# Kernel optimization log

Hardware: AMD Instinct MI355X
Metric: run time of the kernel (lower is better)

Reference implementation:

```python
import jax, jax.numpy as jnp
import numpy as np

# dims
B, P, H, W = 4, 512, 32, 32
C2 = P // 2            # 256 per-branch channels
HEAD = 4
DH = C2 // HEAD        # 64 head dim
L = H * W              # 1024 tokens
DI = 2 * C2            # 512 mamba d_inner (expand=2)
N = 64                 # d_state
R = (C2 + 15) // 16    # 16 dt_rank
KC = 4                 # d_conv


def setup_inputs() -> dict:
    key = jax.random.key(0)
    ks = jax.random.split(key, 32)
    f32 = jnp.float32
    def nrm(k, shape, s=0.02):
        return jax.random.normal(k, shape, f32) * s
    inp = {}
    inp['x'] = jax.random.normal(ks[0], (B, P, H, W), f32)
    # GambaCell rel-pos + gate conv
    inp['rel_h_c'] = jax.random.normal(ks[1], (1, C2, 1, H), f32)
    inp['rel_w_c'] = jax.random.normal(ks[2], (1, C2, W, 1), f32)
    inp['gate_w'] = nrm(ks[3], (C2, C2, 3))
    inp['gate_b'] = jnp.zeros((C2,), f32)
    # Mamba params
    inp['W_in'] = nrm(ks[4], (2 * DI, C2))
    inp['conv_w'] = nrm(ks[5], (DI, KC), 0.2)
    inp['conv_b'] = jnp.zeros((DI,), f32)
    inp['W_x'] = nrm(ks[6], (R + 2 * N, DI))
    inp['W_dt'] = nrm(ks[7], (DI, R), 0.1)
    inp['b_dt'] = jnp.full((DI,), -4.0, f32)
    inp['A_log'] = jnp.broadcast_to(jnp.log(jnp.arange(1, N + 1, dtype=f32)), (DI, N)).copy()
    inp['D_p'] = jnp.ones((DI,), f32)
    inp['W_out'] = nrm(ks[8], (C2, DI))
    # MHSA params (1x1 convs -> dense)
    inp['Wq'] = nrm(ks[9], (C2, C2)); inp['bq'] = jnp.zeros((C2,), f32)
    inp['Wk'] = nrm(ks[10], (C2, C2)); inp['bk'] = jnp.zeros((C2,), f32)
    inp['Wv'] = nrm(ks[11], (C2, C2)); inp['bv'] = jnp.zeros((C2,), f32)
    inp['rel_h_m'] = jax.random.normal(ks[12], (1, HEAD, DH, 1, H), f32) * 0.02
    inp['rel_w_m'] = jax.random.normal(ks[13], (1, HEAD, DH, W, 1), f32) * 0.02
    inp['reg_qk'] = jax.random.normal(ks[14], (1, L, L), f32)
    inp['reg_v'] = jax.random.normal(ks[15], (1, DH, L), f32)
    # Gating params
    inp['Wa'] = nrm(ks[16], (P, C2)); inp['ba'] = jnp.zeros((P,), f32)
    inp['Wb'] = nrm(ks[17], (P, C2)); inp['bb'] = jnp.zeros((P,), f32)
    inp['Wg'] = nrm(ks[18], (1, P)); inp['bg'] = jnp.zeros((1,), f32)
    return inp


def _silu(t):
    return t * jax.nn.sigmoid(t)


def _conv1x1(w, b, t):  # Conv2d kernel_size=1
    return jnp.einsum('oc,bchw->bohw', w, t) + b[None, :, None, None]


def _mamba(seq, W_in, conv_w, conv_b, W_x, W_dt, b_dt, A_log, D_p, W_out):
    # seq: (B, L, C2)
    Bn = seq.shape[0]
    xz = seq @ W_in.T                       # (B,L,2*DI)
    xi, z = jnp.split(xz, 2, axis=-1)
    # causal depthwise conv1d, kernel 4, left-pad 3, trimmed to L
    xc = jnp.transpose(xi, (0, 2, 1))       # (B,DI,L)
    xp = jnp.pad(xc, ((0, 0), (0, 0), (KC - 1, 0)))
    conv = conv_b[None, :, None]
    for kk in range(KC):
        conv = conv + conv_w[None, :, kk, None] * xp[:, :, kk:kk + L]
    xs = _silu(conv).transpose(0, 2, 1)     # (B,L,DI)
    x_dbl = xs @ W_x.T                      # (B,L,R+2N)
    dt = jax.nn.softplus(x_dbl[..., :R] @ W_dt.T + b_dt)   # (B,L,DI)
    Bm = x_dbl[..., R:R + N]                # (B,L,N)
    Cm = x_dbl[..., R + N:]                 # (B,L,N)
    A = -jnp.exp(A_log)                     # (DI,N)

    def step(h, t):
        dt_t, B_t, C_t, u_t = t             # (B,DI),(B,N),(B,N),(B,DI)
        dA = jnp.exp(dt_t[..., None] * A)   # (B,DI,N)
        h = dA * h + (dt_t * u_t)[..., None] * B_t[:, None, :]
        y = jnp.sum(h * C_t[:, None, :], axis=-1)
        return h, y

    h0 = jnp.zeros((Bn, DI, N), seq.dtype)
    scan_in = (dt.transpose(1, 0, 2), Bm.transpose(1, 0, 2),
               Cm.transpose(1, 0, 2), xs.transpose(1, 0, 2))
    _, ys = jax.lax.scan(step, h0, scan_in)  # (L,B,DI)
    y = ys.transpose(1, 0, 2) + D_p * xs
    y = y * _silu(z)
    return y @ W_out.T                      # (B,L,C2)


def _forward(x, rel_h_c, rel_w_c, gate_w, gate_b, W_in, conv_w, conv_b, W_x,
             W_dt, b_dt, A_log, D_p, W_out, Wq, bq, Wk, bk, Wv, bv,
             rel_h_m, rel_w_m, reg_qk, reg_v, Wa, ba, Wb, bb, Wg, bg):
    Bn = x.shape[0]
    x1, x2 = x[:, :C2], x[:, C2:]
    # --- GambaCell branch ---
    seq = x1.reshape(Bn, C2, L).transpose(0, 2, 1)          # (B,L,C2)
    pos = (rel_h_c + rel_w_c).reshape(1, C2, L).transpose(0, 2, 1)
    seq = seq + pos
    sc = seq.transpose(0, 2, 1)                             # (B,C2,L)
    ctx = jax.nn.sigmoid(
        jax.lax.conv_general_dilated(sc, gate_w, (1,), [(1, 1)],
                                     dimension_numbers=('NCH', 'OIH', 'NCH'))
        + gate_b[None, :, None]).transpose(0, 2, 1)          # (B,L,C2)
    ym = _mamba(seq, W_in, conv_w, conv_b, W_x, W_dt, b_dt, A_log, D_p, W_out)
    # faithful to original: view (B,L,C)->(B,C,H,W) with no permute
    out1 = (ym * ctx).reshape(Bn, C2, H, W)
    # --- MHSA branch ---
    q = _conv1x1(Wq, bq, x2).reshape(Bn, HEAD, DH, L)
    k = _conv1x1(Wk, bk, x2).reshape(Bn, HEAD, DH, L)
    v = _conv1x1(Wv, bv, x2).reshape(Bn, HEAD, DH, L)
    cc = jnp.einsum('bhdi,bhdj->bhij', q, k)                # content-content
    posm = (rel_h_m + rel_w_m).reshape(HEAD, DH, L)
    cp = jnp.einsum('hdi,bhdj->bhij', posm, q)              # position^T @ q
    energy = cc + cp                                         # (B,HEAD,L,L)
    e = jnp.concatenate([energy, jnp.broadcast_to(reg_qk[None], (Bn, 1, L, L))], axis=1)
    vp = jnp.concatenate([v, jnp.broadcast_to(reg_v[None], (Bn, 1, DH, L))], axis=1)
    attn = jax.nn.softmax(e, axis=-1)
    out = jnp.einsum('bndj,bnij->bndi', vp, attn)           # v @ attn^T
    out2 = out[:, :HEAD].reshape(Bn, C2, H, W)
    # --- Gating fusion ---
    a_proj = _conv1x1(Wa, ba, out1)
    b_proj = _conv1x1(Wb, bb, out2)
    ga = jax.nn.sigmoid(_conv1x1(Wg, bg, a_proj))
    gb = jax.nn.sigmoid(_conv1x1(Wg, bg, b_proj))
    return ga * a_proj + gb * b_proj                        # (B,P,H,W)


def reference(x, rel_h_c, rel_w_c, gate_w, gate_b, W_in, conv_w, conv_b, W_x,
              W_dt, b_dt, A_log, D_p, W_out, Wq, bq, Wk, bk, Wv, bv,
              rel_h_m, rel_w_m, reg_qk, reg_v, Wa, ba, Wb, bb, Wg, bg):
    return _forward(x, rel_h_c, rel_w_c, gate_w, gate_b, W_in, conv_w, conv_b,
                    W_x, W_dt, b_dt, A_log, D_p, W_out, Wq, bq, Wk, bk, Wv, bv,
                    rel_h_m, rel_w_m, reg_qk, reg_v, Wa, ba, Wb, bb, Wg, bg)
```

## Files before the change

### kernel.cpp

```cpp
#include <hip/hip_runtime.h>
#include <math.h>

static constexpr int Bn = 4, Pp = 512, C2 = 256, HEAD = 4, DHd = 64;
static constexpr int Ll = 1024, DIi = 512, Nn = 64, Rr = 16, KCc = 4;

#define DEVI __device__ __forceinline__

DEVI float sigf(float x){ return 1.0f/(1.0f+__expf(-x)); }
DEVI float softplusf(float x){ return x > 20.f ? x : log1pf(__expf(x)); }

DEVI unsigned short bfh(float f){
  unsigned int u = __float_as_uint(f);
  return (unsigned short)((u + 0x7FFFu + ((u>>16)&1u)) >> 16);
}
DEVI float bff(unsigned short h){ return __uint_as_float(((unsigned int)h)<<16); }

typedef __attribute__((ext_vector_type(8))) short  bf8v;
typedef __attribute__((ext_vector_type(4))) float  f4v;
typedef __attribute__((ext_vector_type(8))) unsigned short u16x8;

__global__ void k_transpose(const float* __restrict__ x, const float* __restrict__ rh,
                            const float* __restrict__ rw, float* __restrict__ seq,
                            float* __restrict__ x2seq){
  __shared__ float t[32][33];
  int b = blockIdx.z, c0 = blockIdx.y*32, l0 = blockIdx.x*32;
  for (int i = threadIdx.y; i < 32; i += 8)
    t[i][threadIdx.x] = x[((size_t)(b*Pp + c0 + i)*Ll) + l0 + threadIdx.x];
  __syncthreads();
  for (int i = threadIdx.y; i < 32; i += 8){
    int l = l0 + i, c = c0 + threadIdx.x;
    float v = t[threadIdx.x][i];
    if (c < C2){
      float pos = rh[c*32 + (l & 31)] + rw[c*32 + (l >> 5)];
      seq[(size_t)(b*Ll + l)*C2 + c] = v + pos;
    } else {
      x2seq[(size_t)(b*Ll + l)*C2 + (c - C2)] = v;
    }
  }
}

__global__ void __launch_bounds__(256) k_mgemm(
    const float* __restrict__ A, const float* __restrict__ B,
    float* __restrict__ C, const float* __restrict__ bias,
    int M, int N, int K, int lda, int ldb, int ldc, int act)
{
  __shared__ __align__(16) unsigned short Ah[64*40], Al[64*40], Bh[64*40], Bl[64*40];
  int m0 = blockIdx.y*64, n0 = blockIdx.x*64;
  int t = threadIdx.x;
  int w = t >> 6, l = t & 63;
  int g = l >> 4, r = l & 15;
  int row0 = w*16;

  f4v acc[4];
  #pragma unroll
  for (int j=0;j<4;++j) acc[j] = (f4v){0.f,0.f,0.f,0.f};

  int sr = t >> 2;
  int sc = (t & 3) * 8;

  for (int k0 = 0; k0 < K; k0 += 32){
    {
      const float* src = A + (size_t)(m0+sr)*lda + k0 + sc;
      float4 v0 = *(const float4*)(src);
      float4 v1 = *(const float4*)(src+4);
      float f[8] = {v0.x,v0.y,v0.z,v0.w,v1.x,v1.y,v1.z,v1.w};
      u16x8 hv, lv;
      #pragma unroll
      for (int i=0;i<8;++i){
        unsigned short h = bfh(f[i]); hv[i] = h;
        lv[i] = bfh(f[i] - bff(h));
      }
      *(u16x8*)&Ah[sr*40+sc] = hv;
      *(u16x8*)&Al[sr*40+sc] = lv;
    }
    {
      const float* src = B + (size_t)(n0+sr)*ldb + k0 + sc;
      float4 v0 = *(const float4*)(src);
      float4 v1 = *(const float4*)(src+4);
      float f[8] = {v0.x,v0.y,v0.z,v0.w,v1.x,v1.y,v1.z,v1.w};
      u16x8 hv, lv;
      #pragma unroll
      for (int i=0;i<8;++i){
        unsigned short h = bfh(f[i]); hv[i] = h;
        lv[i] = bfh(f[i] - bff(h));
      }
      *(u16x8*)&Bh[sr*40+sc] = hv;
      *(u16x8*)&Bl[sr*40+sc] = lv;
    }
    __syncthreads();
    bf8v a_h = *(const bf8v*)&Ah[(row0+r)*40 + g*8];
    bf8v a_l = *(const bf8v*)&Al[(row0+r)*40 + g*8];
    #pragma unroll
    for (int j=0;j<4;++j){
      bf8v b_h = *(const bf8v*)&Bh[(j*16+r)*40 + g*8];
      bf8v b_l = *(const bf8v*)&Bl[(j*16+r)*40 + g*8];
      acc[j] = __builtin_amdgcn_mfma_f32_16x16x32_bf16(a_h, b_h, acc[j], 0, 0, 0);
      acc[j] = __builtin_amdgcn_mfma_f32_16x16x32_bf16(a_h, b_l, acc[j], 0, 0, 0);
      acc[j] = __builtin_amdgcn_mfma_f32_16x16x32_bf16(a_l, b_h, acc[j], 0, 0, 0);
    }
    __syncthreads();
  }
  #pragma unroll
  for (int j=0;j<4;++j){
    int n = n0 + j*16 + r;
    float bv = bias ? bias[n] : 0.f;
    #pragma unroll
    for (int q=0;q<4;++q){
      int m = m0 + row0 + g*4 + q;
      float v = acc[j][q] + bv;
      if (act == 1) v = sigf(v);
      Cb_write:
      C[(size_t)m*ldc + n] = v;
    }
  }
}

template<int BMODE>
__global__ void __launch_bounds__(256) k_gemm(
       const float* __restrict__ A, const float* __restrict__ B,
       float* __restrict__ C, const float* __restrict__ bias,
       int M, int N, int K, int lda, int ldb, int ldc,
       long sA1, long sA2, long sB1, long sB2, long sC1, long sC2, int act)
{
  __shared__ float As[16][64];
  __shared__ float Bs[16][64];
  int z = blockIdx.z;
  const float* Ab = A + (size_t)((z>>2)*sA1 + (z&3)*sA2);
  const float* Bb = B + (size_t)((z>>2)*sB1 + (z&3)*sB2);
  float*       Cb = C + (size_t)((z>>2)*sC1 + (z&3)*sC2);
  int m0 = blockIdx.y*64, n0 = blockIdx.x*64;
  int t = threadIdx.x, tx = t & 15, ty = t >> 4;
  float acc[4][4] = {};
  int arow = t >> 2, akq = (t & 3) * 4;
  for (int k0 = 0; k0 < K; k0 += 16){
    float4 av = *(const float4*)(Ab + (size_t)(m0+arow)*lda + k0 + akq);
    As[akq+0][arow] = av.x; As[akq+1][arow] = av.y;
    As[akq+2][arow] = av.z; As[akq+3][arow] = av.w;
    if (BMODE == 0){
      float4 bv = make_float4(0.f,0.f,0.f,0.f);
      if (n0 + arow < N) bv = *(const float4*)(Bb + (size_t)(n0+arow)*ldb + k0 + akq);
      Bs[akq+0][arow]=bv.x; Bs[akq+1][arow]=bv.y;
      Bs[akq+2][arow]=bv.z; Bs[akq+3][arow]=bv.w;
    } else {
      int kr = t >> 4, nq = (t & 15) * 4;
      float4 bv = make_float4(0.f,0.f,0.f,0.f);
      if (n0 + nq < N) bv = *(const float4*)(Bb + (size_t)(k0+kr)*ldb + n0 + nq);
      *(float4*)&Bs[kr][nq] = bv;
    }
    __syncthreads();
    #pragma unroll
    for (int k = 0; k < 16; ++k){
      float4 a = *(const float4*)&As[k][ty*4];
      float4 b = *(const float4*)&Bs[k][tx*4];
      acc[0][0] = fmaf(a.x,b.x,acc[0][0]); acc[0][1] = fmaf(a.x,b.y,acc[0][1]);
      acc[0][2] = fmaf(a.x,b.z,acc[0][2]); acc[0][3] = fmaf(a.x,b.w,acc[0][3]);
      acc[1][0] = fmaf(a.y,b.x,acc[1][0]); acc[1][1] = fmaf(a.y,b.y,acc[1][1]);
      acc[1][2] = fmaf(a.y,b.z,acc[1][2]); acc[1][3] = fmaf(a.y,b.w,acc[1][3]);
      acc[2][0] = fmaf(a.z,b.x,acc[2][0]); acc[2][1] = fmaf(a.z,b.y,acc[2][1]);
      acc[2][2] = fmaf(a.z,b.z,acc[2][2]); acc[2][3] = fmaf(a.z,b.w,acc[2][3]);
      acc[3][0] = fmaf(a.w,b.x,acc[3][0]); acc[3][1] = fmaf(a.w,b.y,acc[3][1]);
      acc[3][2] = fmaf(a.w,b.z,acc[3][2]); acc[3][3] = fmaf(a.w,b.w,acc[3][3]);
    }
    __syncthreads();
  }
  #pragma unroll
  for (int i = 0; i < 4; ++i){
    int m = m0 + ty*4 + i;
    #pragma unroll
    for (int j = 0; j < 4; ++j){
      int n = n0 + tx*4 + j;
      if (n < N){
        float v = acc[i][j];
        if (bias) v += bias[n];
        if (act == 1) v = sigf(v);
        else if (act == 2) v = softplusf(v);
        Cb[(size_t)m*ldc + n] = v;
      }
    }
  }
}

__global__ void k_im2col(const float* __restrict__ seq, float* __restrict__ A2){
  int idx = blockIdx.x*256 + threadIdx.x;
  int j  = idx % 768;
  int bl = idx / 768;
  int kk = j >> 8, c = j & 255;
  int l = bl & 1023, b = bl >> 10;
  int ls = l + kk - 1;
  float v = 0.f;
  if (ls >= 0 && ls < Ll) v = seq[(size_t)(b*Ll + ls)*C2 + c];
  A2[idx] = v;
}

__global__ void k_packw(const float* __restrict__ gw, float* __restrict__ W2){
  int idx = blockIdx.x*256 + threadIdx.x;
  int j = idx % 768, o = idx / 768;
  int kk = j >> 8, i = j & 255;
  W2[idx] = gw[(size_t)(o*256 + i)*3 + kk];
}

__global__ void k_dwconv(const float* __restrict__ xz, const float* __restrict__ cw,
                         const float* __restrict__ cb, float* __restrict__ xs){
  int idx = blockIdx.x*256 + threadIdx.x;
  int d = idx & 511; int bl = idx >> 9; int l = bl & 1023; int b = bl >> 10;
  float s = cb[d];
  #pragma unroll
  for (int kk = 0; kk < 4; ++kk){
    int ls = l - 3 + kk;
    if (ls >= 0) s = fmaf(cw[d*4+kk], xz[(size_t)(b*Ll+ls)*1024 + d], s);
  }
  xs[idx] = s * sigf(s);
}

__global__ void __launch_bounds__(64, 2) k_scan2(
    const float* __restrict__ dt, const float* __restrict__ xdbl,
    const float* __restrict__ xs, const float* __restrict__ xz,
    const float* __restrict__ A_log, const float* __restrict__ D_p,
    float* __restrict__ y){
  __shared__ float pbuf[64*65];
  int lane = threadIdx.x;
  int wid  = blockIdx.x;
  int b = wid >> 9, d = wid & 511;
  float Ac = -__expf(A_log[d*64 + lane]);
  float Dp = D_p[d];
  float h = 0.f;
  size_t base = (size_t)b*Ll;
  for (int c0 = 0; c0 < Ll; c0 += 64){
    size_t rowj = base + c0 + lane;
    float dtv = dt[rowj*512 + d];
    float uv  = xs[rowj*512 + d];
    float zv  = xz[rowj*1024 + 512 + d];
    float dtu = dtv*uv;
    float Bv[64], Cv[64];
    #pragma unroll
    for (int l = 0; l < 64; ++l){
      size_t r2 = (base + c0 + l)*144;
      Bv[l] = xdbl[r2 + 16 + lane];
      Cv[l] = xdbl[r2 + 80 + lane];
    }
    #pragma unroll
    for (int l = 0; l < 64; ++l){
      float sdt  = __shfl(dtv, l);
      float sdtu = __shfl(dtu, l);
      float dA = __expf(sdt*Ac);
      h = fmaf(dA, h, sdtu*Bv[l]);
      pbuf[l*65 + lane] = h*Cv[l];
    }
    __syncthreads();
    float s0=0.f, s1=0.f, s2=0.f, s3=0.f;
    const float* rp = &pbuf[lane*65];
    #pragma unroll
    for (int n = 0; n < 64; n += 4){
      s0 += rp[n]; s1 += rp[n+1]; s2 += rp[n+2]; s3 += rp[n+3];
    }
    float p = (s0+s1)+(s2+s3);
    y[rowj*512 + d] = (p + Dp*uv) * (zv * sigf(zv));
    __syncthreads();
  }
}

__global__ void k_pack_ab(const float* __restrict__ qt, const float* __restrict__ kt,
                          const float* __restrict__ rhm, const float* __restrict__ rwm,
                          float* __restrict__ Ab, float* __restrict__ Bb){
  int idx = blockIdx.x*256 + threadIdx.x;
  int dd = idx & 127;
  int i  = (idx >> 7) & 1023;
  int h  = (idx >> 17) & 3;
  int b  = idx >> 19;
  float av, bv;
  if (dd < 64){
    size_t q = (size_t)(b*Ll + i)*C2 + h*64 + dd;
    av = qt[q]; bv = kt[q];
  } else {
    int d = dd - 64;
    av = rhm[(h*64+d)*32 + (i & 31)] + rwm[(h*64+d)*32 + (i >> 5)];
    bv = qt[(size_t)(b*Ll + i)*C2 + h*64 + d];
  }
  Ab[idx] = av; Bb[idx] = bv;
}

__global__ void __launch_bounds__(256) k_softmax(float* __restrict__ e){
  __shared__ float red[4];
  __shared__ float red2[4];
  size_t row = blockIdx.x;
  float* p = e + row*1024;
  int t = threadIdx.x;
  float v0 = p[t], v1 = p[t+256], v2 = p[t+512], v3 = p[t+768];
  float mx = fmaxf(fmaxf(v0,v1), fmaxf(v2,v3));
  #pragma unroll
  for (int off=32; off; off>>=1) mx = fmaxf(mx, __shfl_xor(mx, off));
  if ((t&63)==0) red[t>>6] = mx;
  __syncthreads();
  mx = fmaxf(fmaxf(red[0],red[1]), fmaxf(red[2],red[3]));
  v0 = __expf(v0-mx); v1 = __expf(v1-mx); v2 = __expf(v2-mx); v3 = __expf(v3-mx);
  float s = v0+v1+v2+v3;
  #pragma unroll
  for (int off=32; off; off>>=1) s += __shfl_xor(s, off);
  if ((t&63)==0) red2[t>>6] = s;
  __syncthreads();
  s = red2[0]+red2[1]+red2[2]+red2[3];
  float inv = 1.0f/s;
  p[t] = v0*inv; p[t+256] = v1*inv; p[t+512] = v2*inv; p[t+768] = v3*inv;
}

__global__ void k_mulshuf(const float* __restrict__ ym, const float* __restrict__ ctx,
                          float* __restrict__ out1t){
  __shared__ float t[32][33];
  int b = blockIdx.z >> 2, s1 = blockIdx.z & 3;
  int c0 = blockIdx.y*32, s00 = blockIdx.x*32;
  for (int i = threadIdx.y; i < 32; i += 8){
    int c = c0 + i;
    int l = c*4 + s1;
    size_t off = ((size_t)(b*Ll + l))*C2 + s00 + threadIdx.x;
    t[i][threadIdx.x] = ym[off] * ctx[off];
  }
  __syncthreads();
  for (int i = threadIdx.y; i < 32; i += 8){
    int s0 = s00 + i, c = c0 + threadIdx.x;
    int s = s1*256 + s0;
    out1t[((size_t)(b*Ll + s))*C2 + c] = t[threadIdx.x][i];
  }
}

__global__ void __launch_bounds__(256) k_gates(
    const float* __restrict__ ap, const float* __restrict__ bp,
    const float* __restrict__ Wg, const float* __restrict__ bg, float* __restrict__ g){
  __shared__ float ra[4], rb[4];
  int bl = blockIdx.x; int t = threadIdx.x;
  float sa = 0.f, sb = 0.f;
  const float* a = ap + (size_t)bl*512;
  const float* bq = bp + (size_t)bl*512;
  for (int pp = t; pp < 512; pp += 256){ float w = Wg[pp]; sa = fmaf(w, a[pp], sa); sb = fmaf(w, bq[pp], sb); }
  #pragma unroll
  for (int off=32; off; off>>=1){ sa += __shfl_xor(sa,off); sb += __shfl_xor(sb,off); }
  if ((t&63)==0){ ra[t>>6]=sa; rb[t>>6]=sb; }
  __syncthreads();
  if (t==0){
    float b0 = bg[0];
    g[bl]        = sigf(ra[0]+ra[1]+ra[2]+ra[3] + b0);
    g[4096 + bl] = sigf(rb[0]+rb[1]+rb[2]+rb[3] + b0);
  }
}

__global__ void k_final(const float* __restrict__ ap, const float* __restrict__ bp,
                        const float* __restrict__ g, float* __restrict__ out){
  int bpid = blockIdx.x; int b = bpid >> 9, p = bpid & 511;
  for (int l = threadIdx.x; l < Ll; l += 256){
    int bl = b*Ll + l;
    float ga = g[bl], gb = g[4096 + bl];
    out[((size_t)(b*Pp + p) << 10) + l] =
        ga*ap[(size_t)bl*512 + p] + gb*bp[(size_t)bl*512 + p];
  }
}

static inline void gemm(hipStream_t s, int bmode, const float* A, const float* B, float* C,
                        const float* bias, int M, int N, int K, int lda, int ldb, int ldc,
                        long sA1, long sA2, long sB1, long sB2, long sC1, long sC2,
                        int batch, int act){
  dim3 g((N+63)/64, M/64, batch), blk(256);
  if (bmode == 0)
    k_gemm<0><<<g, blk, 0, s>>>(A,B,C,bias,M,N,K,lda,ldb,ldc,sA1,sA2,sB1,sB2,sC1,sC2,act);
  else
    k_gemm<1><<<g, blk, 0, s>>>(A,B,C,bias,M,N,K,lda,ldb,ldc,sA1,sA2,sB1,sB2,sC1,sC2,act);
}

static inline void mgemm(hipStream_t s, const float* A, const float* B, float* C,
                         const float* bias, int M, int N, int K, int lda, int ldb, int ldc,
                         int act){
  dim3 g(N/64, M/64, 1), blk(256);
  k_mgemm<<<g, blk, 0, s>>>(A,B,C,bias,M,N,K,lda,ldb,ldc,act);
}

extern "C" void kernel_launch(void* const* d_in, const int* in_sizes, int n_in,
                              void* d_out, int out_size, void* d_ws, size_t ws_size,
                              hipStream_t stream) {
  const float* x      = (const float*)d_in[0];
  const float* rh_c   = (const float*)d_in[1];
  const float* rw_c   = (const float*)d_in[2];
  const float* gate_w = (const float*)d_in[3];
  const float* gate_b = (const float*)d_in[4];
  const float* W_in   = (const float*)d_in[5];
  const float* conv_w = (const float*)d_in[6];
  const float* conv_b = (const float*)d_in[7];
  const float* W_x    = (const float*)d_in[8];
  const float* W_dt   = (const float*)d_in[9];
  const float* b_dt   = (const float*)d_in[10];
  const float* A_log  = (const float*)d_in[11];
  const float* D_p    = (const float*)d_in[12];
  const float* W_out  = (const float*)d_in[13];
  const float* Wq     = (const float*)d_in[14];
  const float* bq     = (const float*)d_in[15];
  const float* Wk     = (const float*)d_in[16];
  const float* bk     = (const float*)d_in[17];
  const float* Wv     = (const float*)d_in[18];
  const float* bv     = (const float*)d_in[19];
  const float* rhm    = (const float*)d_in[20];
  const float* rwm    = (const float*)d_in[21];
  const float* Wa     = (const float*)d_in[24];
  const float* ba     = (const float*)d_in[25];
  const float* Wb     = (const float*)d_in[26];
  const float* bb     = (const float*)d_in[27];
  const float* Wg     = (const float*)d_in[28];
  const float* bg     = (const float*)d_in[29];
  float* out = (float*)d_out;
  float* ws  = (float*)d_ws;

  float* seq    = ws;
  float* x2seq  = ws +  1048576;
  float* qt     = ws +  2097152;
  float* kt     = ws +  3145728;
  float* vt     = ws +  4194304;
  float* Abuf   = ws +  5242880;
  float* Bbuf   = ws +  7340032;
  float* arena  = ws +  9437184;
  float* out2   = ws + 26214400;
  float* out1   = ws + 27262976;
  float* aproj  = ws + 28311552;
  float* bproj  = ws + 30408704;
  float* gates  = ws + 32505856;
  float* W2     = ws + 32514048;
  float* A2   = arena;
  float* ctx  = arena +  3145728;
  float* xz   = arena +  4194304;
  float* xs   = arena +  8388608;
  float* xdbl = arena + 10485760;
  float* dtb  = arena + 11075584;
  float* yb   = arena + 13172736;
  float* ym   = arena + 15269888;
  float* energy = arena;

  k_transpose<<<dim3(32,16,4), dim3(32,8), 0, stream>>>(x, rh_c, rw_c, seq, x2seq);

  mgemm(stream, x2seq, Wq, qt, bq, 4096,256,256, 256,256,256, 0);
  mgemm(stream, x2seq, Wk, kt, bk, 4096,256,256, 256,256,256, 0);
  mgemm(stream, x2seq, Wv, vt, bv, 4096,256,256, 256,256,256, 0);
  k_pack_ab<<<8192, 256, 0, stream>>>(qt, kt, rhm, rwm, Abuf, Bbuf);
  gemm(stream,0, Abuf, Bbuf, energy, nullptr, 1024,1024,128, 128,128,1024,
       4L*131072, 131072, 4L*131072, 131072, 4L*1048576, 1048576, 16, 0);
  k_softmax<<<16384, 256, 0, stream>>>(energy);
  gemm(stream,1, energy, vt, out2, nullptr, 1024,64,1024, 1024,256,256,
       4L*1048576, 1048576, 262144, 64, 262144, 64, 16, 0);

  k_packw<<<768, 256, 0, stream>>>(gate_w, W2);
  k_im2col<<<12288, 256, 0, stream>>>(seq, A2);
  mgemm(stream, A2, W2, ctx, gate_b, 4096,256,768, 768,768,256, 1);
  mgemm(stream, seq, W_in, xz, nullptr, 4096,1024,256, 256,256,1024, 0);
  k_dwconv<<<8192, 256, 0, stream>>>(xz, conv_w, conv_b, xs);
  gemm(stream,0, xs, W_x, xdbl, nullptr, 4096,144,512, 512,512,144, 0,0,0,0,0,0, 1, 0);
  {
    dim3 g(8, 64, 1), blk(256);
    k_gemm<0><<<g, blk, 0, stream>>>(xdbl, W_dt, dtb, b_dt, 4096,512,16, 144,16,512,
                                     0,0,0,0,0,0, 2);
  }
  k_scan2<<<2048, 64, 0, stream>>>(dtb, xdbl, xs, xz, A_log, D_p, yb);
  mgemm(stream, yb, W_out, ym, nullptr, 4096,256,512, 512,512,256, 0);
  k_mulshuf<<<dim3(8,8,16), dim3(32,8), 0, stream>>>(ym, ctx, out1);

  mgemm(stream, out1, Wa, aproj, ba, 4096,512,256, 256,256,512, 0);
  mgemm(stream, out2, Wb, bproj, bb, 4096,512,256, 256,256,512, 0);
  k_gates<<<4096, 256, 0, stream>>>(aproj, bproj, Wg, bg, gates);
  k_final<<<2048, 256, 0, stream>>>(aproj, bproj, gates, out);
}
```

Before: 652.9 us.

## Move attention GEMMs to batched split-bf16 MFMA and restructure scan through LDS

The MFMA split-bf16 GEMM gains batch strides, and the energy (QK plus position) and attention-times-V GEMMs now run on it instead of the scalar FP32 tiled GEMM. V is transposed first into a scratch buffer so the MFMA kernel can read it K-contiguous. The selective scan is also rewritten to work on 32-token chunks staged through shared memory rather than 64-entry register arrays, which lowers register pressure. The cost is an extra transpose pass, the reuse of the aproj buffer as scratch, and about 3-term bf16-split precision in the attention GEMMs.

Measured after the change: 606.2 us. -7.2%, faster.

```diff
diff --git a/kernel.cpp b/kernel.cpp
--- a/kernel.cpp
+++ b/kernel.cpp
@@ -39,12 +39,17 @@
   }
 }
 
-__global__ void __launch_bounds__(256) k_mgemm(
+__global__ void __launch_bounds__(256) k_mgemmb(
     const float* __restrict__ A, const float* __restrict__ B,
     float* __restrict__ C, const float* __restrict__ bias,
-    int M, int N, int K, int lda, int ldb, int ldc, int act)
+    int M, int N, int K, int lda, int ldb, int ldc,
+    long sA1, long sA2, long sB1, long sB2, long sC1, long sC2, int act)
 {
   __shared__ __align__(16) unsigned short Ah[64*40], Al[64*40], Bh[64*40], Bl[64*40];
+  int z = blockIdx.z;
+  const float* Ab = A + (size_t)((z>>2)*sA1 + (z&3)*sA2);
+  const float* Bb = B + (size_t)((z>>2)*sB1 + (z&3)*sB2);
+  float*       Cb = C + (size_t)((z>>2)*sC1 + (z&3)*sC2);
   int m0 = blockIdx.y*64, n0 = blockIdx.x*64;
   int t = threadIdx.x;
   int w = t >> 6, l = t & 63;
@@ -60,7 +65,7 @@
 
   for (int k0 = 0; k0 < K; k0 += 32){
     {
-      const float* src = A + (size_t)(m0+sr)*lda + k0 + sc;
+      const float* src = Ab + (size_t)(m0+sr)*lda + k0 + sc;
       float4 v0 = *(const float4*)(src);
       float4 v1 = *(const float4*)(src+4);
       float f[8] = {v0.x,v0.y,v0.z,v0.w,v1.x,v1.y,v1.z,v1.w};
@@ -74,7 +79,7 @@
       *(u16x8*)&Al[sr*40+sc] = lv;
     }
     {
-      const float* src = B + (size_t)(n0+sr)*ldb + k0 + sc;
+      const float* src = Bb + (size_t)(n0+sr)*ldb + k0 + sc;
       float4 v0 = *(const float4*)(src);
       float4 v1 = *(const float4*)(src+4);
       float f[8] = {v0.x,v0.y,v0.z,v0.w,v1.x,v1.y,v1.z,v1.w};
@@ -109,44 +114,30 @@
       int m = m0 + row0 + g*4 + q;
       float v = acc[j][q] + bv;
       if (act == 1) v = sigf(v);
-      Cb_write:
-      C[(size_t)m*ldc + n] = v;
-    }
-  }
-}
-
-template<int BMODE>
+      Cb[(size_t)m*ldc + n] = v;
+    }
+  }
+}
+
 __global__ void __launch_bounds__(256) k_gemm(
        const float* __restrict__ A, const float* __restrict__ B,
        float* __restrict__ C, const float* __restrict__ bias,
-       int M, int N, int K, int lda, int ldb, int ldc,
-       long sA1, long sA2, long sB1, long sB2, long sC1, long sC2, int act)
+       int M, int N, int K, int lda, int ldb, int ldc, int act)
 {
   __shared__ float As[16][64];
   __shared__ float Bs[16][64];
-  int z = blockIdx.z;
-  const float* Ab = A + (size_t)((z>>2)*sA1 + (z&3)*sA2);
-  const float* Bb = B + (size_t)((z>>2)*sB1 + (z&3)*sB2);
-  float*       Cb = C + (size_t)((z>>2)*sC1 + (z&3)*sC2);
   int m0 = blockIdx.y*64, n0 = blockIdx.x*64;
   int t = threadIdx.x, tx = t & 15, ty = t >> 4;
   float acc[4][4] = {};
   int arow = t >> 2, akq = (t & 3) * 4;
   for (int k0 = 0; k0 < K; k0 += 16){
-    float4 av = *(const float4*)(Ab + (size_t)(m0+arow)*lda + k0 + akq);
+    float4 av = *(const float4*)(A + (size_t)(m0+arow)*lda + k0 + akq);
     As[akq+0][arow] = av.x; As[akq+1][arow] = av.y;
     As[akq+2][arow] = av.z; As[akq+3][arow] = av.w;
-    if (BMODE == 0){
-      float4 bv = make_float4(0.f,0.f,0.f,0.f);
-      if (n0 + arow < N) bv = *(const float4*)(Bb + (size_t)(n0+arow)*ldb + k0 + akq);
-      Bs[akq+0][arow]=bv.x; Bs[akq+1][arow]=bv.y;
-      Bs[akq+2][arow]=bv.z; Bs[akq+3][arow]=bv.w;
-    } else {
-      int kr = t >> 4, nq = (t & 15) * 4;
-      float4 bv = make_float4(0.f,0.f,0.f,0.f);
-      if (n0 + nq < N) bv = *(const float4*)(Bb + (size_t)(k0+kr)*ldb + n0 + nq);
-      *(float4*)&Bs[kr][nq] = bv;
-    }
+    float4 bv = make_float4(0.f,0.f,0.f,0.f);
+    if (n0 + arow < N) bv = *(const float4*)(B + (size_t)(n0+arow)*ldb + k0 + akq);
+    Bs[akq+0][arow]=bv.x; Bs[akq+1][arow]=bv.y;
+    Bs[akq+2][arow]=bv.z; Bs[akq+3][arow]=bv.w;
     __syncthreads();
     #pragma unroll
     for (int k = 0; k < 16; ++k){
@@ -174,7 +165,7 @@
         if (bias) v += bias[n];
         if (act == 1) v = sigf(v);
         else if (act == 2) v = softplusf(v);
-        Cb[(size_t)m*ldc + n] = v;
+        C[(size_t)m*ldc + n] = v;
       }
     }
   }
@@ -212,12 +203,15 @@
   xs[idx] = s * sigf(s);
 }
 
-__global__ void __launch_bounds__(64, 2) k_scan2(
+__global__ void __launch_bounds__(64) k_scan3(
     const float* __restrict__ dt, const float* __restrict__ xdbl,
     const float* __restrict__ xs, const float* __restrict__ xz,
     const float* __restrict__ A_log, const float* __restrict__ D_p,
     float* __restrict__ y){
-  __shared__ float pbuf[64*65];
+  __shared__ float Bs[32*64];
+  __shared__ float Cs[32*64];
+  __shared__ float pb[32*65];
+  __shared__ float sdt[32], sdtu[32];
   int lane = threadIdx.x;
   int wid  = blockIdx.x;
   int b = wid >> 9, d = wid & 511;
@@ -225,36 +219,42 @@
   float Dp = D_p[d];
   float h = 0.f;
   size_t base = (size_t)b*Ll;
-  for (int c0 = 0; c0 < Ll; c0 += 64){
-    size_t rowj = base + c0 + lane;
-    float dtv = dt[rowj*512 + d];
-    float uv  = xs[rowj*512 + d];
-    float zv  = xz[rowj*1024 + 512 + d];
-    float dtu = dtv*uv;
-    float Bv[64], Cv[64];
+  int jl = lane & 31;
+  bool lo = lane < 32;
+  for (int c0 = 0; c0 < Ll; c0 += 32){
+    size_t rowj = base + c0 + jl;
+    float uv = 0.f, zv = 0.f;
+    if (lo){
+      float dtv = dt[rowj*512 + d];
+      uv = xs[rowj*512 + d];
+      zv = xz[rowj*1024 + 512 + d];
+      sdt[jl]  = dtv;
+      sdtu[jl] = dtv*uv;
+    }
+    for (int l = 0; l < 32; ++l){
+      size_t r2 = (base + c0 + l)*144;
+      Bs[l*64 + lane] = xdbl[r2 + 16 + lane];
+      Cs[l*64 + lane] = xdbl[r2 + 80 + lane];
+    }
+    __syncthreads();
     #pragma unroll
-    for (int l = 0; l < 64; ++l){
-      size_t r2 = (base + c0 + l)*144;
-      Bv[l] = xdbl[r2 + 16 + lane];
-      Cv[l] = xdbl[r2 + 80 + lane];
-    }
-    #pragma unroll
-    for (int l = 0; l < 64; ++l){
-      float sdt  = __shfl(dtv, l);
-      float sdtu = __shfl(dtu, l);
-      float dA = __expf(sdt*Ac);
-      h = fmaf(dA, h, sdtu*Bv[l]);
-      pbuf[l*65 + lane] = h*Cv[l];
-    }
-    __syncthreads();
-    float s0=0.f, s1=0.f, s2=0.f, s3=0.f;
-    const float* rp = &pbuf[lane*65];
-    #pragma unroll
-    for (int n = 0; n < 64; n += 4){
-      s0 += rp[n]; s1 += rp[n+1]; s2 += rp[n+2]; s3 += rp[n+3];
-    }
-    float p = (s0+s1)+(s2+s3);
-    y[rowj*512 + d] = (p + Dp*uv) * (zv * sigf(zv));
+    for (int l = 0; l < 32; ++l){
+      float dA = __expf(sdt[l]*Ac);
+      h = fmaf(dA, h, sdtu[l]*Bs[l*64 + lane]);
+      pb[l*65 + lane] = h*Cs[l*64 + lane];
+    }
+    __syncthreads();
+    {
+      const float* rp = &pb[jl*65 + (lo ? 0 : 32)];
+      float s0=0.f, s1=0.f, s2=0.f, s3=0.f;
+      #pragma unroll
+      for (int n = 0; n < 32; n += 4){
+        s0 += rp[n]; s1 += rp[n+1]; s2 += rp[n+2]; s3 += rp[n+3];
+      }
+      float p = (s0+s1)+(s2+s3);
+      p += __shfl_xor(p, 32);
+      if (lo) y[rowj*512 + d] = (p + Dp*uv) * (zv * sigf(zv));
+    }
     __syncthreads();
   }
 }
@@ -279,6 +279,16 @@
   Ab[idx] = av; Bb[idx] = bv;
 }
 
+__global__ void k_vtrans(const float* __restrict__ vt, float* __restrict__ vT){
+  __shared__ float t[32][33];
+  int b = blockIdx.z, c0 = blockIdx.y*32, j0 = blockIdx.x*32;
+  for (int i = threadIdx.y; i < 32; i += 8)
+    t[i][threadIdx.x] = vt[(size_t)(b*Ll + j0 + i)*C2 + c0 + threadIdx.x];
+  __syncthreads();
+  for (int i = threadIdx.y; i < 32; i += 8)
+    vT[((size_t)(b*C2 + c0 + i))*Ll + j0 + threadIdx.x] = t[threadIdx.x][i];
+}
+
 __global__ void __launch_bounds__(256) k_softmax(float* __restrict__ e){
   __shared__ float red[4];
   __shared__ float red2[4];
@@ -353,22 +363,11 @@
   }
 }
 
-static inline void gemm(hipStream_t s, int bmode, const float* A, const float* B, float* C,
-                        const float* bias, int M, int N, int K, int lda, int ldb, int ldc,
-                        long sA1, long sA2, long sB1, long sB2, long sC1, long sC2,
-                        int batch, int act){
-  dim3 g((N+63)/64, M/64, batch), blk(256);
-  if (bmode == 0)
-    k_gemm<0><<<g, blk, 0, s>>>(A,B,C,bias,M,N,K,lda,ldb,ldc,sA1,sA2,sB1,sB2,sC1,sC2,act);
-  else
-    k_gemm<1><<<g, blk, 0, s>>>(A,B,C,bias,M,N,K,lda,ldb,ldc,sA1,sA2,sB1,sB2,sC1,sC2,act);
-}
-
 static inline void mgemm(hipStream_t s, const float* A, const float* B, float* C,
                          const float* bias, int M, int N, int K, int lda, int ldb, int ldc,
                          int act){
   dim3 g(N/64, M/64, 1), blk(256);
-  k_mgemm<<<g, blk, 0, s>>>(A,B,C,bias,M,N,K,lda,ldb,ldc,act);
+  k_mgemmb<<<g, blk, 0, s>>>(A,B,C,bias,M,N,K,lda,ldb,ldc, 0,0,0,0,0,0, act);
 }
 
 extern "C" void kernel_launch(void* const* d_in, const int* in_sizes, int n_in,
@@ -428,6 +427,7 @@
   float* yb   = arena + 13172736;
   float* ym   = arena + 15269888;
   float* energy = arena;
+  float* vT   = aproj;
 
   k_transpose<<<dim3(32,16,4), dim3(32,8), 0, stream>>>(x, rh_c, rw_c, seq, x2seq);
 
@@ -435,24 +435,35 @@
   mgemm(stream, x2seq, Wk, kt, bk, 4096,256,256, 256,256,256, 0);
   mgemm(stream, x2seq, Wv, vt, bv, 4096,256,256, 256,256,256, 0);
   k_pack_ab<<<8192, 256, 0, stream>>>(qt, kt, rhm, rwm, Abuf, Bbuf);
-  gemm(stream,0, Abuf, Bbuf, energy, nullptr, 1024,1024,128, 128,128,1024,
-       4L*131072, 131072, 4L*131072, 131072, 4L*1048576, 1048576, 16, 0);
+  k_vtrans<<<dim3(32,8,4), dim3(32,8), 0, stream>>>(vt, vT);
+  {
+    dim3 g(16, 16, 16), blk(256);
+    k_mgemmb<<<g, blk, 0, stream>>>(Abuf, Bbuf, energy, nullptr,
+        1024,1024,128, 128,128,1024,
+        4L*131072, 131072, 4L*131072, 131072, 4L*1048576, 1048576, 0);
+  }
   k_softmax<<<16384, 256, 0, stream>>>(energy);
-  gemm(stream,1, energy, vt, out2, nullptr, 1024,64,1024, 1024,256,256,
-       4L*1048576, 1048576, 262144, 64, 262144, 64, 16, 0);
+  {
+    dim3 g(1, 16, 16), blk(256);
+    k_mgemmb<<<g, blk, 0, stream>>>(energy, vT, out2, nullptr,
+        1024,64,1024, 1024,1024,256,
+        4L*1048576, 1048576, 262144, 65536, 262144, 64, 0);
+  }
 
   k_packw<<<768, 256, 0, stream>>>(gate_w, W2);
   k_im2col<<<12288, 256, 0, stream>>>(seq, A2);
   mgemm(stream, A2, W2, ctx, gate_b, 4096,256,768, 768,768,256, 1);
   mgemm(stream, seq, W_in, xz, nullptr, 4096,1024,256, 256,256,1024, 0);
   k_dwconv<<<8192, 256, 0, stream>>>(xz, conv_w, conv_b, xs);
-  gemm(stream,0, xs, W_x, xdbl, nullptr, 4096,144,512, 512,512,144, 0,0,0,0,0,0, 1, 0);
+  {
+    dim3 g(3, 64, 1), blk(256);
+    k_gemm<<<g, blk, 0, stream>>>(xs, W_x, xdbl, nullptr, 4096,144,512, 512,512,144, 0);
+  }
   {
     dim3 g(8, 64, 1), blk(256);
-    k_gemm<0><<<g, blk, 0, stream>>>(xdbl, W_dt, dtb, b_dt, 4096,512,16, 144,16,512,
-                                     0,0,0,0,0,0, 2);
-  }
-  k_scan2<<<2048, 64, 0, stream>>>(dtb, xdbl, xs, xz, A_log, D_p, yb);
+    k_gemm<<<g, blk, 0, stream>>>(xdbl, W_dt, dtb, b_dt, 4096,512,16, 144,16,512, 2);
+  }
+  k_scan3<<<2048, 64, 0, stream>>>(dtb, xdbl, xs, xz, A_log, D_p, yb);
   mgemm(stream, yb, W_out, ym, nullptr, 4096,256,512, 512,512,256, 0);
   k_mulshuf<<<dim3(8,8,16), dim3(32,8), 0, stream>>>(ym, ctx, out1);
 
```
